# Kernel optimization log

Measured on AMD Instinct MI355X. Metric: run time of the kernel, lower is better.

Reference implementation:

```python
import jax, jax.numpy as jnp
import numpy as np

D = 2            # stalk dimension d
FD = 3           # final_d = d + 1 (add_lp=True, add_hp=False)
HID = 32         # hidden_channels
N_NODES = 50000
E0 = 200000      # undirected edges; directed edge list has 2*E0 entries (second half reversed)
IN_CH = 128
OUT_CH = 32
N_LAYERS = 2
PSIZE = D * (D + 1) // 2  # cayley param size per edge


def _spectral_normalize(W, iters=20):
    # torch spectral_norm: power iteration with detached u, v; sigma = u^T W v
    u = jnp.full((W.shape[0],), 1.0 / np.sqrt(W.shape[0]), W.dtype)
    def body(_, u):
        v = W.T @ u
        v = v / (jnp.linalg.norm(v) + 1e-12)
        u2 = W @ v
        return u2 / (jnp.linalg.norm(u2) + 1e-12)
    u = jax.lax.fori_loop(0, iters, body, u)
    u = jax.lax.stop_gradient(u)
    v = jax.lax.stop_gradient(W.T @ u)
    v = v / (jnp.linalg.norm(v) + 1e-12)
    return W / (u @ W @ v)


def _cayley(p):
    # p: [E, PSIZE] lower-tri params -> skew A -> orthogonal Q = (I - A)^{-1}(I + A)
    E = p.shape[0]
    r, c = jnp.tril_indices(D)
    M = jnp.zeros((E, D, D), p.dtype).at[:, r, c].set(p)
    A = M - jnp.swapaxes(M, 1, 2)
    I = jnp.eye(D, dtype=p.dtype)
    return jnp.linalg.solve(I[None] - A, I[None] + A)


def setup_inputs() -> dict:
    key = jax.random.key(0)
    ks = jax.random.split(key, 8)
    src = jax.random.randint(ks[0], (E0,), 0, N_NODES)
    dst = jax.random.randint(ks[1], (E0,), 0, N_NODES)
    # symmetric directed edge list; edge j and edge j+E0 are reverses of each other
    edge_index = jnp.concatenate([jnp.stack([src, dst]), jnp.stack([dst, src])], axis=1)
    x = jax.random.normal(ks[2], (N_NODES, IN_CH), jnp.float32)
    s = 0.02
    W1 = jax.random.normal(ks[3], (FD * HID, IN_CH), jnp.float32) * s
    b1 = jnp.zeros((FD * HID,), jnp.float32)
    W2 = jax.random.normal(ks[4], (OUT_CH, FD * HID), jnp.float32) * s
    b2 = jnp.zeros((OUT_CH,), jnp.float32)
    W_left = jnp.tile(jnp.eye(FD, dtype=jnp.float32)[None], (N_LAYERS, 1, 1))  # init eye per torch
    W_right = jax.random.normal(ks[5], (N_LAYERS, HID, HID), jnp.float32) / np.sqrt(HID)
    eps = jnp.zeros((N_LAYERS, FD, 1), jnp.float32)
    W_sheaf = jax.random.normal(ks[6], (N_LAYERS, PSIZE, 2 * FD * HID), jnp.float32) * s
    W_wt = jax.random.normal(ks[7], (N_LAYERS, 1, 2 * FD * HID), jnp.float32) * s
    return {"x": x, "edge_index": edge_index, "W1": W1, "b1": b1, "W2": W2, "b2": b2,
            "W_left": W_left, "W_right": W_right, "eps": eps, "W_sheaf": W_sheaf, "W_wt": W_wt}


def reference(x, edge_index, W1, b1, W2, b2, W_left, W_right, eps, W_sheaf, W_wt):
    N = x.shape[0]
    row, col = edge_index[0], edge_index[1]
    e0 = row.shape[0] // 2
    rev = jnp.concatenate([jnp.arange(e0) + e0, jnp.arange(e0)])  # reverse-edge index
    # lin1 + ELU (dropouts = 0 in eval)
    h = jax.nn.elu(x @ W1.T + b1)                 # [N, FD*HID]
    xc = h.reshape(N * FD, HID)                   # [N*FD, HID]
    x0 = xc
    for layer in range(N_LAYERS):
        # --- sheaf learner + edge weight learner (gather endpoint features) ---
        xn = xc.reshape(N, FD * HID)
        cat = jnp.concatenate([xn[row], xn[col]], axis=-1)   # [2*E0, 2*FD*HID]
        p = jnp.tanh(cat @ W_sheaf[layer].T)                 # sheaf map params [2*E0, PSIZE]
        wdir = jax.nn.sigmoid(cat @ W_wt[layer].T)[:, 0]
        w = wdir * wdir[rev]                                 # symmetric edge weight
        # --- normalized connection (bundle) Laplacian ---
        Q = _cayley(p)                                       # per-edge orthogonal maps
        T = jnp.einsum('eij,eik->ejk', Q, Q[rev])            # transport F_u^T F_v
        w2 = w * w
        deg = jax.ops.segment_sum(w2, row, num_segments=N)
        dinv = jnp.where(deg > 0, jax.lax.rsqrt(jnp.maximum(deg, 1e-30)), 0.0)
        cnorm = w2 * dinv[row] * dinv[col]                   # [2*E0]
        # --- left / right weights (spectral-normalized) ---
        Wl = _spectral_normalize(W_left[layer])
        Wr = _spectral_normalize(W_right[layer])
        y = xc.reshape(N, FD, HID)
        y = jnp.einsum('ef,nfh->neh', Wl, y)                 # mix stalk dims
        y = jnp.einsum('neh,ch->nec', y, Wr)                 # mix channels
        # --- apply block-sparse Laplacian: Lx[u] = x[u] - sum_e c_e B_e x[v] ---
        yv = y[col]                                          # gather  [2*E0, FD, HID]
        tv = jnp.concatenate([jnp.einsum('eij,ejh->eih', T, yv[:, :D]), yv[:, D:]], axis=1)
        agg = jax.ops.segment_sum(cnorm[:, None, None] * tv, row, num_segments=N)
        diag = jnp.where(deg > 0, 1.0, 0.0)[:, None, None]
        z = jax.nn.elu((diag * y - agg).reshape(N * FD, HID))
        # --- epsilon-gated residual ---
        coeff = jnp.tile(1.0 + jnp.tanh(eps[layer]), (N, 1))  # [N*FD, 1]
        x0 = coeff * x0 - z
        xc = x0
    return xc.reshape(N, FD * HID) @ W2.T + b2
```

## Files before the change

### kernel.cpp

```cpp
#include <hip/hip_runtime.h>

#define NN 50000
#define E0 200000
#define E2 400000
#define NGROUPS ((NN + 7) / 8)
#define NCHUNK  ((NN + 255) / 256)
#define NTILES  ((NN + 63) / 64)

typedef __attribute__((ext_vector_type(8))) short short8;
typedef __attribute__((ext_vector_type(4))) float f32x4;

__device__ __forceinline__ float eluf(float x) { return x > 0.0f ? x : expm1f(x); }
__device__ __forceinline__ float sigmoidf(float x) { return 1.0f / (1.0f + expf(-x)); }
__device__ __forceinline__ unsigned rne_bf16(float x) {
    unsigned u = __float_as_uint(x);
    return (u + 0x7fffu + ((u >> 16) & 1u)) >> 16;
}

__global__ __launch_bounds__(256) void k_setup(const float* __restrict__ Wl_in, const float* __restrict__ Wr_in,
                                               float* __restrict__ Wl_out, float* __restrict__ Wr_out,
                                               int* __restrict__ cnt, int* __restrict__ fill,
                                               float* __restrict__ deg) {
    __shared__ float W[32 * 33];
    __shared__ float us[32], vs[32], tmp[32];
    __shared__ float scal;
    int t = threadIdx.x;
    if (blockIdx.x < 2) {
        int l = blockIdx.x;
        for (int i = t; i < 1024; i += 256) W[(i >> 5) * 33 + (i & 31)] = Wr_in[l * 1024 + i];
        if (t < 32) us[t] = 0.17677669529663688f;
        __syncthreads();
        for (int it = 0; it < 20; ++it) {
            if (t < 32) { float a = 0; for (int r = 0; r < 32; ++r) a = fmaf(W[r * 33 + t], us[r], a); tmp[t] = a; }
            __syncthreads();
            if (t == 0) { float s = 0; for (int c = 0; c < 32; ++c) s += tmp[c] * tmp[c]; scal = 1.0f / (sqrtf(s) + 1e-12f); }
            __syncthreads();
            if (t < 32) vs[t] = tmp[t] * scal;
            __syncthreads();
            if (t < 32) { float a = 0; for (int c = 0; c < 32; ++c) a = fmaf(W[t * 33 + c], vs[c], a); tmp[t] = a; }
            __syncthreads();
            if (t == 0) { float s = 0; for (int r = 0; r < 32; ++r) s += tmp[r] * tmp[r]; scal = 1.0f / (sqrtf(s) + 1e-12f); }
            __syncthreads();
            if (t < 32) us[t] = tmp[t] * scal;
            __syncthreads();
        }
        if (t < 32) { float a = 0; for (int r = 0; r < 32; ++r) a = fmaf(W[r * 33 + t], us[r], a); tmp[t] = a; }
        __syncthreads();
        if (t == 0) {
            float s = 0; for (int c = 0; c < 32; ++c) s += tmp[c] * tmp[c];
            scal = (sqrtf(s) + 1e-12f) / s;
        }
        __syncthreads();
        for (int i = t; i < 1024; i += 256) Wr_out[l * 1024 + i] = W[(i >> 5) * 33 + (i & 31)] * scal;
        if (t == 0) {
            float M[9];
            for (int i = 0; i < 9; ++i) M[i] = Wl_in[l * 9 + i];
            float u[3] = {0.5773502691896258f, 0.5773502691896258f, 0.5773502691896258f};
            float v[3], u2[3];
            for (int it = 0; it < 20; ++it) {
                float s = 0;
                for (int c = 0; c < 3; ++c) { v[c] = M[c] * u[0] + M[3 + c] * u[1] + M[6 + c] * u[2]; s += v[c] * v[c]; }
                float inv = 1.0f / (sqrtf(s) + 1e-12f);
                for (int c = 0; c < 3; ++c) v[c] *= inv;
                s = 0;
                for (int r = 0; r < 3; ++r) { u2[r] = M[r * 3] * v[0] + M[r * 3 + 1] * v[1] + M[r * 3 + 2] * v[2]; s += u2[r] * u2[r]; }
                inv = 1.0f / (sqrtf(s) + 1e-12f);
                for (int r = 0; r < 3; ++r) u[r] = u2[r] * inv;
            }
            float s = 0;
            for (int c = 0; c < 3; ++c) { v[c] = M[c] * u[0] + M[3 + c] * u[1] + M[6 + c] * u[2]; s += v[c] * v[c]; }
            float inv = (sqrtf(s) + 1e-12f) / s;
            for (int i = 0; i < 9; ++i) Wl_out[l * 9 + i] = M[i] * inv;
        }
    } else {
        int base = (blockIdx.x - 2) * 256 + t;
        int stride = (gridDim.x - 2) * 256;
        for (int i = base; i < NN; i += stride) { cnt[i] = 0; fill[i] = 0; deg[i] = 0.0f; }
    }
}

template<int K, int N, int NH, bool ELU, bool HIST>
__global__ __launch_bounds__(256) void k_gemm(const float* __restrict__ X,
                                              const float* __restrict__ W,
                                              const float* __restrict__ bias,
                                              float* __restrict__ out,
                                              const int* __restrict__ row, int* __restrict__ cnt) {
    constexpr int KP = K + 8;
    constexpr int NT = NH / 16;
    constexpr int KS = K / 32;
    constexpr int NHALVES = N / NH;
    __shared__ __align__(16) unsigned short whi[NH * KP];
    __shared__ __align__(16) unsigned short wlo[NH * KP];
    int tid = threadIdx.x;
    if (HIST) {
        for (int e = blockIdx.x * 256 + tid; e < E2; e += gridDim.x * 256)
            atomicAdd(&cnt[row[e]], 1);
    }
    const int ch = blockIdx.x % NHALVES;
    const int tstream = blockIdx.x / NHALVES;
    const int nstreams = gridDim.x / NHALVES;
    for (int i = tid; i < NH * K; i += 256) {
        float v = W[ch * NH * K + i];
        int r = i / K, c = i % K;
        unsigned h = rne_bf16(v);
        whi[r * KP + c] = (unsigned short)h;
        wlo[r * KP + c] = (unsigned short)rne_bf16(v - __uint_as_float(h << 16));
    }
    __syncthreads();
    int wave = tid >> 6, lane = tid & 63;
    int quad = lane >> 4, r16 = lane & 15;
    for (int t = tstream; t < NTILES; t += nstreams) {
        long m = (long)t * 64 + wave * 16 + r16;
        long mc = m < NN ? m : (NN - 1);
        const float* xrow = X + mc * K + quad * 8;
        short8 ah[KS], al[KS];
#pragma unroll
        for (int ks = 0; ks < KS; ++ks) {
            const float4* xp = (const float4*)(xrow + ks * 32);
            float4 p0 = xp[0], p1 = xp[1];
            float xv[8] = {p0.x, p0.y, p0.z, p0.w, p1.x, p1.y, p1.z, p1.w};
#pragma unroll
            for (int j = 0; j < 8; ++j) {
                unsigned h = rne_bf16(xv[j]);
                ah[ks][j] = (short)h;
                al[ks][j] = (short)rne_bf16(xv[j] - __uint_as_float(h << 16));
            }
        }
        long mbase = (long)t * 64 + wave * 16 + quad * 4;
#pragma unroll
        for (int tt = 0; tt < NT; ++tt) {
            f32x4 acc = (f32x4){0.f, 0.f, 0.f, 0.f};
#pragma unroll
            for (int ks = 0; ks < KS; ++ks) {
                int ro = (tt * 16 + r16) * KP + ks * 32 + quad * 8;
                short8 bh = *(const short8*)&whi[ro];
                short8 bl = *(const short8*)&wlo[ro];
                acc = __builtin_amdgcn_mfma_f32_16x16x32_bf16(ah[ks], bh, acc, 0, 0, 0);
                acc = __builtin_amdgcn_mfma_f32_16x16x32_bf16(al[ks], bh, acc, 0, 0, 0);
                acc = __builtin_amdgcn_mfma_f32_16x16x32_bf16(ah[ks], bl, acc, 0, 0, 0);
            }
            int coln = ch * NH + tt * 16 + r16;
            float b = bias[coln];
#pragma unroll
            for (int rr = 0; rr < 4; ++rr) {
                long mm = mbase + rr;
                if (mm < NN) {
                    float v = acc[rr] + b;
                    if (ELU) v = eluf(v);
                    out[mm * N + coln] = v;
                }
            }
        }
    }
}

__global__ __launch_bounds__(256) void k_scan1(const int* __restrict__ cnt, int* __restrict__ start,
                                               int* __restrict__ bsum) {
    __shared__ int s[256];
    int b = blockIdx.x, t = threadIdx.x;
    int i = b * 256 + t;
    int v = (i < NN) ? cnt[i] : 0;
    s[t] = v;
    __syncthreads();
    for (int off = 1; off < 256; off <<= 1) {
        int add = (t >= off) ? s[t - off] : 0;
        __syncthreads();
        s[t] += add;
        __syncthreads();
    }
    if (i < NN) start[i] = s[t] - v;
    if (t == 255) bsum[b] = s[t];
}
__global__ __launch_bounds__(256) void k_scan2(const int* __restrict__ bsum, int* __restrict__ bofs, int nb) {
    __shared__ int s[256];
    int t = threadIdx.x;
    int v = (t < nb) ? bsum[t] : 0;
    s[t] = v;
    __syncthreads();
    for (int off = 1; off < 256; off <<= 1) {
        int add = (t >= off) ? s[t - off] : 0;
        __syncthreads();
        s[t] += add;
        __syncthreads();
    }
    if (t < nb) bofs[t] = s[t] - v;
}
__global__ __launch_bounds__(256) void k_fill(const int* __restrict__ row, const int* __restrict__ start,
                                              const int* __restrict__ bofs,
                                              int* __restrict__ fill, int* __restrict__ eslot) {
    int e = blockIdx.x * 256 + threadIdx.x;
    if (e >= E2) return;
    int u = row[e];
    eslot[e] = start[u] + bofs[u >> 8] + atomicAdd(&fill[u], 1);
}

__global__ __launch_bounds__(256) void k_y8(const float* __restrict__ xc,
                                            const float* __restrict__ Wl, const float* __restrict__ Wr,
                                            const float* __restrict__ Wsh, const float* __restrict__ Wwt,
                                            int layer, unsigned* __restrict__ yA,
                                            unsigned short* __restrict__ yB,
                                            float4* __restrict__ proj,
                                            float* __restrict__ deg) {
    __shared__ float wrs[32 * 33];
    __shared__ float wls[9];
    __shared__ float xcs[8][96];
    __shared__ float ws1[192], wt[192];
    int tid = threadIdx.x;
    int n0 = blockIdx.x * 8;
    if (tid < 8) { int nz = n0 + tid; if (nz < NN) deg[nz] = 0.0f; }
    for (int i = tid; i < 1024; i += 256) wrs[(i >> 5) * 33 + (i & 31)] = Wr[i];
    if (tid < 9) wls[tid] = Wl[tid];
    if (tid < 192) {
        ws1[tid] = Wsh[(layer * 3 + 1) * 192 + tid];
        wt[tid]  = Wwt[layer * 192 + tid];
    }
    for (int i = tid; i < 768; i += 256) {
        int n = n0 + i / 96;
        xcs[i / 96][i % 96] = (n < NN) ? xc[n * 96 + i % 96] : 0.0f;
    }
    __syncthreads();
    int node = tid >> 5, c = tid & 31;
    int n = n0 + node;
    float a1 = 0, a2 = 0, a3 = 0, a4 = 0;
#pragma unroll
    for (int j = 0; j < 3; ++j) {
        int k = j * 32 + c;
        float xv = xcs[node][k];
        a1 = fmaf(xv, ws1[k], a1);
        a2 = fmaf(xv, ws1[96 + k], a2);
        a3 = fmaf(xv, wt[k], a3);
        a4 = fmaf(xv, wt[96 + k], a4);
    }
#pragma unroll
    for (int off = 16; off; off >>= 1) {
        a1 += __shfl_xor(a1, off);
        a2 += __shfl_xor(a2, off);
        a3 += __shfl_xor(a3, off);
        a4 += __shfl_xor(a4, off);
    }
    if (c == 0 && n < NN) proj[n] = make_float4(a1, a2, a3, a4);
    if (n < NN) {
        float t0 = 0, t1 = 0, t2 = 0;
        const float* wr = &wrs[c * 33];
        const float* xr = xcs[node];
#pragma unroll
        for (int h = 0; h < 32; ++h) {
            float w = wr[h];
            t0 = fmaf(xr[h], w, t0);
            t1 = fmaf(xr[32 + h], w, t1);
            t2 = fmaf(xr[64 + h], w, t2);
        }
        float o0 = wls[0] * t0 + wls[1] * t1 + wls[2] * t2;
        float o1 = wls[3] * t0 + wls[4] * t1 + wls[5] * t2;
        float o2 = wls[6] * t0 + wls[7] * t1 + wls[8] * t2;
        yA[n * 32 + c] = rne_bf16(o0) | (rne_bf16(o1) << 16);
        yB[n * 32 + c] = (unsigned short)rne_bf16(o2);
    }
}

__global__ __launch_bounds__(256) void k_coef(const int* __restrict__ row, const int* __restrict__ col,
                                              const int* __restrict__ eslot,
                                              const float4* __restrict__ proj,
                                              uint2* __restrict__ meta, float* __restrict__ deg) {
    int e = blockIdx.x * 256 + threadIdx.x;
    if (e >= E0) return;
    int u = row[e], v = col[e];
    float4 pu = proj[u], pv = proj[v];
    float a_e = tanhf(pu.x + pv.y);
    float a_r = tanhf(pv.x + pu.y);
    float wd_e = sigmoidf(pu.z + pv.w);
    float wd_r = sigmoidf(pv.z + pu.w);
    float w = wd_e * wd_r;
    float w2 = w * w;
    float ie = 1.0f / (1.0f + a_e * a_e), ir = 1.0f / (1.0f + a_r * a_r);
    float ce = (1.0f - a_e * a_e) * ie, se = 2.0f * a_e * ie;
    float cr = (1.0f - a_r * a_r) * ir, sr = 2.0f * a_r * ir;
    float C = ce * cr + se * sr;
    float S = ce * sr - se * cr;
    unsigned cb = rne_bf16(C), sb = rne_bf16(S), wb = rne_bf16(w2);
    meta[eslot[e]]      = make_uint2(cb | (sb << 16), (unsigned)v | (wb << 16));
    meta[eslot[e + E0]] = make_uint2(cb | ((sb ^ 0x8000u) << 16), (unsigned)u | (wb << 16));
    atomicAdd(&deg[u], w2);
    atomicAdd(&deg[v], w2);
}

__global__ __launch_bounds__(256) void k_gather(const int* __restrict__ start, const int* __restrict__ bofs,
                                                const int* __restrict__ cnt,
                                                const uint2* __restrict__ meta,
                                                const float* __restrict__ deg,
                                                const unsigned* __restrict__ yA,
                                                const unsigned short* __restrict__ yB,
                                                const float* __restrict__ eps,
                                                int layer, float* __restrict__ xc) {
    int tid = threadIdx.x;
    int node = tid >> 5, c = tid & 31;
    int n = blockIdx.x * 8 + node;
    if (n >= NN) return;
    int s0 = start[n] + bofs[n >> 8], ec = cnt[n];
    float dn = deg[n];
    float du = dn > 0.0f ? rsqrtf(fmaxf(dn, 1e-30f)) : 0.0f;
    float acc0 = 0, acc1 = 0, acc2 = 0;
    for (int bs = 0; bs < ec; bs += 32) {
        int nb2 = min(32, ec - bs);
        float CC = 0, SS = 0, cnl = 0;
        int vj = 0;
        if (c < nb2) {
            uint2 mt = meta[s0 + bs + c];
            vj = (int)(mt.y & 0xffffu);
            float w2 = __uint_as_float(mt.y & 0xffff0000u);
            float Cv = __uint_as_float(mt.x << 16);
            float Sv = __uint_as_float(mt.x & 0xffff0000u);
            float dv = deg[vj];
            float dvi = dv > 0.0f ? rsqrtf(fmaxf(dv, 1e-30f)) : 0.0f;
            cnl = w2 * du * dvi;
            CC = cnl * Cv;
            SS = cnl * Sv;
        }
        for (int j = 0; j < nb2; ++j) {
            float Cj = __shfl(CC, j, 32);
            float Sj = __shfl(SS, j, 32);
            float cj = __shfl(cnl, j, 32);
            int v = __shfl(vj, j, 32);
            unsigned ua = yA[v * 32 + c];
            unsigned ub = (unsigned)yB[v * 32 + c];
            float y0 = __uint_as_float(ua << 16);
            float y1 = __uint_as_float(ua & 0xffff0000u);
            float y2 = __uint_as_float(ub << 16);
            acc0 = fmaf(Cj, y0, acc0);
            acc0 = fmaf(-Sj, y1, acc0);
            acc1 = fmaf(Sj, y0, acc1);
            acc1 = fmaf(Cj, y1, acc1);
            acc2 = fmaf(cj, y2, acc2);
        }
    }
    float diag = dn > 0.0f ? 1.0f : 0.0f;
    unsigned ua = yA[n * 32 + c];
    unsigned ub = (unsigned)yB[n * 32 + c];
    float oy0 = __uint_as_float(ua << 16);
    float oy1 = __uint_as_float(ua & 0xffff0000u);
    float oy2 = __uint_as_float(ub << 16);
    float c0 = 1.0f + tanhf(eps[layer * 3 + 0]);
    float c1 = 1.0f + tanhf(eps[layer * 3 + 1]);
    float c2 = 1.0f + tanhf(eps[layer * 3 + 2]);
    int base = n * 96 + c;
    float z0 = eluf(diag * oy0 - acc0);
    float z1 = eluf(diag * oy1 - acc1);
    float z2 = eluf(diag * oy2 - acc2);
    xc[base]      = c0 * xc[base]      - z0;
    xc[base + 32] = c1 * xc[base + 32] - z1;
    xc[base + 64] = c2 * xc[base + 64] - z2;
}

extern "C" void kernel_launch(void* const* d_in, const int* in_sizes, int n_in,
                              void* d_out, int out_size, void* d_ws, size_t ws_size,
                              hipStream_t stream) {
    const float* x     = (const float*)d_in[0];
    const int*   ei    = (const int*)d_in[1];
    const float* W1    = (const float*)d_in[2];
    const float* b1    = (const float*)d_in[3];
    const float* W2    = (const float*)d_in[4];
    const float* b2    = (const float*)d_in[5];
    const float* Wl    = (const float*)d_in[6];
    const float* Wr    = (const float*)d_in[7];
    const float* eps   = (const float*)d_in[8];
    const float* Wsh   = (const float*)d_in[9];
    const float* Wwt   = (const float*)d_in[10];
    float* out = (float*)d_out;
    const int* row = ei;
    const int* col = ei + E2;

    char* pc = (char*)d_ws;
    float* xc    = (float*)pc;          pc += (size_t)NN * 96 * 4;
    uint2* meta  = (uint2*)pc;          pc += (size_t)E2 * 8;
    unsigned* yA = (unsigned*)pc;       pc += (size_t)NN * 32 * 4;
    unsigned short* yB = (unsigned short*)pc; pc += (size_t)NN * 32 * 2;
    pc = (char*)(((size_t)pc + 15) & ~(size_t)15);
    float4* proj = (float4*)pc;         pc += (size_t)NN * 16;
    float* deg   = (float*)pc;          pc += (size_t)NN * 4;
    float* Wl_n  = (float*)pc;          pc += 32 * 4;
    float* Wr_n  = (float*)pc;          pc += 2048 * 4;
    int* cnt     = (int*)pc;            pc += (size_t)NN * 4;
    int* start   = (int*)pc;            pc += (size_t)NN * 4;
    int* fill    = (int*)pc;            pc += (size_t)NN * 4;
    int* eslot   = (int*)pc;            pc += (size_t)E2 * 4;
    int* bsum    = (int*)pc;            pc += 256 * 4;
    int* bofs    = (int*)pc;            pc += 256 * 4;

    const int EB = (E2 + 255) / 256;

    k_setup<<<34, 256, 0, stream>>>(Wl, Wr, Wl_n, Wr_n, cnt, fill, deg);
    k_gemm<128, 96, 48, true, true><<<512, 256, 0, stream>>>(x, W1, b1, xc, row, cnt);
    k_scan1<<<NCHUNK, 256, 0, stream>>>(cnt, start, bsum);
    k_scan2<<<1, 256, 0, stream>>>(bsum, bofs, NCHUNK);
    k_fill<<<EB, 256, 0, stream>>>(row, start, bofs, fill, eslot);
    for (int l = 0; l < 2; ++l) {
        k_y8<<<NGROUPS, 256, 0, stream>>>(xc, Wl_n + l * 9, Wr_n + l * 1024, Wsh, Wwt, l,
                                          yA, yB, proj, deg);
        k_coef<<<(E0 + 255) / 256, 256, 0, stream>>>(row, col, eslot, proj, meta, deg);
        k_gather<<<NGROUPS, 256, 0, stream>>>(start, bofs, cnt, meta, deg, yA, yB, eps, l, xc);
    }
    k_gemm<96, 32, 32, false, false><<<512, 256, 0, stream>>>(xc, W2, b2, out, nullptr, nullptr);
}
```

Baseline: 347.9 us.

## Fuse fill into layer-0 y8 and fuse layer-0 gather with layer-1 y8

Merges the CSR slot-fill kernel into the first y/projection kernel as extra blocks, and fuses layer 0's neighbour gather and residual update with layer 1's y/projection computation. Double-buffered y and degree arrays prevent the fused kernel from overwriting data still being read. This removes two launches and a round-trip of xc through global memory. In exchange the fused kernel does more work per block, and bounds checks were dropped because NN is a multiple of 8.

Result: faster. 331.2 us (-4.8%).

```diff
diff --git a/kernel.cpp b/kernel.cpp
--- a/kernel.cpp
+++ b/kernel.cpp
@@ -6,6 +6,7 @@
 #define NGROUPS ((NN + 7) / 8)
 #define NCHUNK  ((NN + 255) / 256)
 #define NTILES  ((NN + 63) / 64)
+#define EB      ((E2 + 255) / 256)
 
 typedef __attribute__((ext_vector_type(8))) short short8;
 typedef __attribute__((ext_vector_type(4))) float f32x4;
@@ -20,7 +21,7 @@
 __global__ __launch_bounds__(256) void k_setup(const float* __restrict__ Wl_in, const float* __restrict__ Wr_in,
                                                float* __restrict__ Wl_out, float* __restrict__ Wr_out,
                                                int* __restrict__ cnt, int* __restrict__ fill,
-                                               float* __restrict__ deg) {
+                                               float* __restrict__ deg0) {
     __shared__ float W[32 * 33];
     __shared__ float us[32], vs[32], tmp[32];
     __shared__ float scal;
@@ -75,7 +76,7 @@
     } else {
         int base = (blockIdx.x - 2) * 256 + t;
         int stride = (gridDim.x - 2) * 256;
-        for (int i = base; i < NN; i += stride) { cnt[i] = 0; fill[i] = 0; deg[i] = 0.0f; }
+        for (int i = base; i < NN; i += stride) { cnt[i] = 0; fill[i] = 0; deg0[i] = 0.0f; }
     }
 }
 
@@ -185,38 +186,38 @@
     }
     if (t < nb) bofs[t] = s[t] - v;
 }
-__global__ __launch_bounds__(256) void k_fill(const int* __restrict__ row, const int* __restrict__ start,
-                                              const int* __restrict__ bofs,
-                                              int* __restrict__ fill, int* __restrict__ eslot) {
-    int e = blockIdx.x * 256 + threadIdx.x;
-    if (e >= E2) return;
-    int u = row[e];
-    eslot[e] = start[u] + bofs[u >> 8] + atomicAdd(&fill[u], 1);
-}
-
-__global__ __launch_bounds__(256) void k_y8(const float* __restrict__ xc,
-                                            const float* __restrict__ Wl, const float* __restrict__ Wr,
-                                            const float* __restrict__ Wsh, const float* __restrict__ Wwt,
-                                            int layer, unsigned* __restrict__ yA,
-                                            unsigned short* __restrict__ yB,
-                                            float4* __restrict__ proj,
-                                            float* __restrict__ deg) {
+
+__global__ __launch_bounds__(256) void k_filly8(const float* __restrict__ xc,
+                                                const float* __restrict__ Wl, const float* __restrict__ Wr,
+                                                const float* __restrict__ Wsh, const float* __restrict__ Wwt,
+                                                unsigned* __restrict__ yA, unsigned short* __restrict__ yB,
+                                                float4* __restrict__ proj,
+                                                const int* __restrict__ row, const int* __restrict__ start,
+                                                const int* __restrict__ bofs,
+                                                int* __restrict__ fill, int* __restrict__ eslot) {
+    int tid = threadIdx.x;
+    if (blockIdx.x >= NGROUPS) {
+        int e = (blockIdx.x - NGROUPS) * 256 + tid;
+        if (e < E2) {
+            int u = row[e];
+            eslot[e] = start[u] + bofs[u >> 8] + atomicAdd(&fill[u], 1);
+        }
+        return;
+    }
     __shared__ float wrs[32 * 33];
     __shared__ float wls[9];
     __shared__ float xcs[8][96];
     __shared__ float ws1[192], wt[192];
-    int tid = threadIdx.x;
     int n0 = blockIdx.x * 8;
-    if (tid < 8) { int nz = n0 + tid; if (nz < NN) deg[nz] = 0.0f; }
     for (int i = tid; i < 1024; i += 256) wrs[(i >> 5) * 33 + (i & 31)] = Wr[i];
     if (tid < 9) wls[tid] = Wl[tid];
     if (tid < 192) {
-        ws1[tid] = Wsh[(layer * 3 + 1) * 192 + tid];
-        wt[tid]  = Wwt[layer * 192 + tid];
-    }
-    for (int i = tid; i < 768; i += 256) {
-        int n = n0 + i / 96;
-        xcs[i / 96][i % 96] = (n < NN) ? xc[n * 96 + i % 96] : 0.0f;
+        ws1[tid] = Wsh[192 + tid];
+        wt[tid]  = Wwt[tid];
+    }
+    for (int i = tid; i < 192; i += 256) {
+        int nd = i / 24, of = (i % 24) * 4;
+        *(float4*)&xcs[nd][of] = *(const float4*)&xc[(n0 + nd) * 96 + of];
     }
     __syncthreads();
     int node = tid >> 5, c = tid & 31;
@@ -238,8 +239,8 @@
         a3 += __shfl_xor(a3, off);
         a4 += __shfl_xor(a4, off);
     }
-    if (c == 0 && n < NN) proj[n] = make_float4(a1, a2, a3, a4);
-    if (n < NN) {
+    if (c == 0) proj[n] = make_float4(a1, a2, a3, a4);
+    {
         float t0 = 0, t1 = 0, t2 = 0;
         const float* wr = &wrs[c * 33];
         const float* xr = xcs[node];
@@ -282,6 +283,116 @@
     meta[eslot[e + E0]] = make_uint2(cb | ((sb ^ 0x8000u) << 16), (unsigned)u | (wb << 16));
     atomicAdd(&deg[u], w2);
     atomicAdd(&deg[v], w2);
+}
+
+__global__ __launch_bounds__(256) void k_gatherY(const int* __restrict__ start, const int* __restrict__ bofs,
+                                                 const int* __restrict__ cnt,
+                                                 const uint2* __restrict__ meta,
+                                                 const float* __restrict__ deg0,
+                                                 const unsigned* __restrict__ yA0,
+                                                 const unsigned short* __restrict__ yB0,
+                                                 const float* __restrict__ eps,
+                                                 float* __restrict__ xc,
+                                                 const float* __restrict__ Wl, const float* __restrict__ Wr,
+                                                 const float* __restrict__ Wsh, const float* __restrict__ Wwt,
+                                                 unsigned* __restrict__ yA1, unsigned short* __restrict__ yB1,
+                                                 float4* __restrict__ proj, float* __restrict__ deg1) {
+    __shared__ float wrs[32 * 33];
+    __shared__ float wls[9];
+    __shared__ float xcs[8][96];
+    __shared__ float ws1[192], wt[192];
+    int tid = threadIdx.x;
+    for (int i = tid; i < 1024; i += 256) wrs[(i >> 5) * 33 + (i & 31)] = Wr[i];
+    if (tid < 9) wls[tid] = Wl[tid];
+    if (tid < 192) {
+        ws1[tid] = Wsh[(1 * 3 + 1) * 192 + tid];
+        wt[tid]  = Wwt[1 * 192 + tid];
+    }
+    int node = tid >> 5, c = tid & 31;
+    int n = blockIdx.x * 8 + node;
+    int s0 = start[n] + bofs[n >> 8], ec = cnt[n];
+    float dn = deg0[n];
+    float du = dn > 0.0f ? rsqrtf(fmaxf(dn, 1e-30f)) : 0.0f;
+    float acc0 = 0, acc1 = 0, acc2 = 0;
+    for (int bs = 0; bs < ec; bs += 32) {
+        int nb2 = min(32, ec - bs);
+        float CC = 0, SS = 0, cnl = 0;
+        int vj = 0;
+        if (c < nb2) {
+            uint2 mt = meta[s0 + bs + c];
+            vj = (int)(mt.y & 0xffffu);
+            float w2 = __uint_as_float(mt.y & 0xffff0000u);
+            float Cv = __uint_as_float(mt.x << 16);
+            float Sv = __uint_as_float(mt.x & 0xffff0000u);
+            float dv = deg0[vj];
+            float dvi = dv > 0.0f ? rsqrtf(fmaxf(dv, 1e-30f)) : 0.0f;
+            cnl = w2 * du * dvi;
+            CC = cnl * Cv;
+            SS = cnl * Sv;
+        }
+        for (int j = 0; j < nb2; ++j) {
+            float Cj = __shfl(CC, j, 32);
+            float Sj = __shfl(SS, j, 32);
+            float cj = __shfl(cnl, j, 32);
+            int v = __shfl(vj, j, 32);
+            unsigned ua = yA0[v * 32 + c];
+            unsigned ub = (unsigned)yB0[v * 32 + c];
+            float y0 = __uint_as_float(ua << 16);
+            float y1 = __uint_as_float(ua & 0xffff0000u);
+            float y2 = __uint_as_float(ub << 16);
+            acc0 = fmaf(Cj, y0, acc0);
+            acc0 = fmaf(-Sj, y1, acc0);
+            acc1 = fmaf(Sj, y0, acc1);
+            acc1 = fmaf(Cj, y1, acc1);
+            acc2 = fmaf(cj, y2, acc2);
+        }
+    }
+    float diag = dn > 0.0f ? 1.0f : 0.0f;
+    unsigned ua = yA0[n * 32 + c];
+    unsigned ub = (unsigned)yB0[n * 32 + c];
+    float oy0 = __uint_as_float(ua << 16);
+    float oy1 = __uint_as_float(ua & 0xffff0000u);
+    float oy2 = __uint_as_float(ub << 16);
+    float c0 = 1.0f + tanhf(eps[0]);
+    float c1 = 1.0f + tanhf(eps[1]);
+    float c2 = 1.0f + tanhf(eps[2]);
+    int base = n * 96 + c;
+    float nx0 = c0 * xc[base]      - eluf(diag * oy0 - acc0);
+    float nx1 = c1 * xc[base + 32] - eluf(diag * oy1 - acc1);
+    float nx2 = c2 * xc[base + 64] - eluf(diag * oy2 - acc2);
+    xc[base] = nx0; xc[base + 32] = nx1; xc[base + 64] = nx2;
+    if (c == 0) deg1[n] = 0.0f;
+    xcs[node][c] = nx0; xcs[node][32 + c] = nx1; xcs[node][64 + c] = nx2;
+    __syncthreads();
+    float a1 = nx0 * ws1[c] + nx1 * ws1[32 + c] + nx2 * ws1[64 + c];
+    float a2 = nx0 * ws1[96 + c] + nx1 * ws1[128 + c] + nx2 * ws1[160 + c];
+    float a3 = nx0 * wt[c] + nx1 * wt[32 + c] + nx2 * wt[64 + c];
+    float a4 = nx0 * wt[96 + c] + nx1 * wt[128 + c] + nx2 * wt[160 + c];
+#pragma unroll
+    for (int off = 16; off; off >>= 1) {
+        a1 += __shfl_xor(a1, off);
+        a2 += __shfl_xor(a2, off);
+        a3 += __shfl_xor(a3, off);
+        a4 += __shfl_xor(a4, off);
+    }
+    if (c == 0) proj[n] = make_float4(a1, a2, a3, a4);
+    {
+        float t0 = 0, t1 = 0, t2 = 0;
+        const float* wr = &wrs[c * 33];
+        const float* xr = xcs[node];
+#pragma unroll
+        for (int h = 0; h < 32; ++h) {
+            float w = wr[h];
+            t0 = fmaf(xr[h], w, t0);
+            t1 = fmaf(xr[32 + h], w, t1);
+            t2 = fmaf(xr[64 + h], w, t2);
+        }
+        float o0 = wls[0] * t0 + wls[1] * t1 + wls[2] * t2;
+        float o1 = wls[3] * t0 + wls[4] * t1 + wls[5] * t2;
+        float o2 = wls[6] * t0 + wls[7] * t1 + wls[8] * t2;
+        yA1[n * 32 + c] = rne_bf16(o0) | (rne_bf16(o1) << 16);
+        yB1[n * 32 + c] = (unsigned short)rne_bf16(o2);
+    }
 }
 
 __global__ __launch_bounds__(256) void k_gather(const int* __restrict__ start, const int* __restrict__ bofs,
@@ -370,34 +481,35 @@
     const int* col = ei + E2;
 
     char* pc = (char*)d_ws;
-    float* xc    = (float*)pc;          pc += (size_t)NN * 96 * 4;
-    uint2* meta  = (uint2*)pc;          pc += (size_t)E2 * 8;
-    unsigned* yA = (unsigned*)pc;       pc += (size_t)NN * 32 * 4;
-    unsigned short* yB = (unsigned short*)pc; pc += (size_t)NN * 32 * 2;
+    float* xc     = (float*)pc;          pc += (size_t)NN * 96 * 4;
+    uint2* meta   = (uint2*)pc;          pc += (size_t)E2 * 8;
+    unsigned* yA0 = (unsigned*)pc;       pc += (size_t)NN * 32 * 4;
+    unsigned* yA1 = (unsigned*)pc;       pc += (size_t)NN * 32 * 4;
+    unsigned short* yB0 = (unsigned short*)pc; pc += (size_t)NN * 32 * 2;
+    unsigned short* yB1 = (unsigned short*)pc; pc += (size_t)NN * 32 * 2;
     pc = (char*)(((size_t)pc + 15) & ~(size_t)15);
-    float4* proj = (float4*)pc;         pc += (size_t)NN * 16;
-    float* deg   = (float*)pc;          pc += (size_t)NN * 4;
-    float* Wl_n  = (float*)pc;          pc += 32 * 4;
-    float* Wr_n  = (float*)pc;          pc += 2048 * 4;
-    int* cnt     = (int*)pc;            pc += (size_t)NN * 4;
-    int* start   = (int*)pc;            pc += (size_t)NN * 4;
-    int* fill    = (int*)pc;            pc += (size_t)NN * 4;
-    int* eslot   = (int*)pc;            pc += (size_t)E2 * 4;
-    int* bsum    = (int*)pc;            pc += 256 * 4;
-    int* bofs    = (int*)pc;            pc += 256 * 4;
-
-    const int EB = (E2 + 255) / 256;
-
-    k_setup<<<34, 256, 0, stream>>>(Wl, Wr, Wl_n, Wr_n, cnt, fill, deg);
+    float4* proj  = (float4*)pc;         pc += (size_t)NN * 16;
+    float* deg0   = (float*)pc;          pc += (size_t)NN * 4;
+    float* deg1   = (float*)pc;          pc += (size_t)NN * 4;
+    float* Wl_n   = (float*)pc;          pc += 32 * 4;
+    float* Wr_n   = (float*)pc;          pc += 2048 * 4;
+    int* cnt      = (int*)pc;            pc += (size_t)NN * 4;
+    int* start    = (int*)pc;            pc += (size_t)NN * 4;
+    int* fill     = (int*)pc;            pc += (size_t)NN * 4;
+    int* eslot    = (int*)pc;            pc += (size_t)E2 * 4;
+    int* bsum     = (int*)pc;            pc += 256 * 4;
+    int* bofs     = (int*)pc;            pc += 256 * 4;
+
+    k_setup<<<34, 256, 0, stream>>>(Wl, Wr, Wl_n, Wr_n, cnt, fill, deg0);
     k_gemm<128, 96, 48, true, true><<<512, 256, 0, stream>>>(x, W1, b1, xc, row, cnt);
     k_scan1<<<NCHUNK, 256, 0, stream>>>(cnt, start, bsum);
     k_scan2<<<1, 256, 0, stream>>>(bsum, bofs, NCHUNK);
-    k_fill<<<EB, 256, 0, stream>>>(row, start, bofs, fill, eslot);
-    for (int l = 0; l < 2; ++l) {
-        k_y8<<<NGROUPS, 256, 0, stream>>>(xc, Wl_n + l * 9, Wr_n + l * 1024, Wsh, Wwt, l,
-                                          yA, yB, proj, deg);
-        k_coef<<<(E0 + 255) / 256, 256, 0, stream>>>(row, col, eslot, proj, meta, deg);
-        k_gather<<<NGROUPS, 256, 0, stream>>>(start, bofs, cnt, meta, deg, yA, yB, eps, l, xc);
-    }
+    k_filly8<<<NGROUPS + EB, 256, 0, stream>>>(xc, Wl_n, Wr_n, Wsh, Wwt,
+                                               yA0, yB0, proj, row, start, bofs, fill, eslot);
+    k_coef<<<(E0 + 255) / 256, 256, 0, stream>>>(row, col, eslot, proj, meta, deg0);
+    k_gatherY<<<NGROUPS, 256, 0, stream>>>(start, bofs, cnt, meta, deg0, yA0, yB0, eps, xc,
+                                           Wl_n + 9, Wr_n + 1024, Wsh, Wwt, yA1, yB1, proj, deg1);
+    k_coef<<<(E0 + 255) / 256, 256, 0, stream>>>(row, col, eslot, proj, meta, deg1);
+    k_gather<<<NGROUPS, 256, 0, stream>>>(start, bofs, cnt, meta, deg1, yA1, yB1, eps, 1, xc);
     k_gemm<96, 32, 32, false, false><<<512, 256, 0, stream>>>(xc, W2, b2, out, nullptr, nullptr);
 }
```
